# Optimization experiments

Hardware: AMD Instinct MI355X
Metric: run time of the kernel (lower is better)

Reference implementation:

```python
import jax, jax.numpy as jnp
import numpy as np

B, S, D, H = 1, 4096, 768, 12
HD = D // H
FF = 4 * D
EPS = 1e-5


def _layer_norm(x, w, b):
    mu = jnp.mean(x, axis=-1, keepdims=True)
    var = jnp.mean((x - mu) ** 2, axis=-1, keepdims=True)
    return (x - mu) * jax.lax.rsqrt(var + EPS) * w + b


def setup_inputs() -> dict:
    key = jax.random.key(0)
    ks = jax.random.split(key, 16)
    s = 0.02
    inp = {
        "hidden_states": jax.random.normal(ks[0], (B, S, D), jnp.float32),
        "attention_mask": jnp.ones((B, S), jnp.int32),
        "ln1_w": jnp.ones((D,), jnp.float32),
        "ln1_b": jnp.zeros((D,), jnp.float32),
        "wq": jax.random.normal(ks[1], (D, D), jnp.float32) * s,
        "bq": jnp.zeros((D,), jnp.float32),
        "wk": jax.random.normal(ks[2], (D, D), jnp.float32) * s,
        "bk": jnp.zeros((D,), jnp.float32),
        "wv": jax.random.normal(ks[3], (D, D), jnp.float32) * s,
        "bv": jnp.zeros((D,), jnp.float32),
        "wo": jax.random.normal(ks[4], (D, D), jnp.float32) * s,
        "bo": jnp.zeros((D,), jnp.float32),
        "ln2_w": jnp.ones((D,), jnp.float32),
        "ln2_b": jnp.zeros((D,), jnp.float32),
        "w_up": jax.random.normal(ks[5], (D, FF), jnp.float32) * s,
        "b_up": jnp.zeros((FF,), jnp.float32),
        "w_down": jax.random.normal(ks[6], (FF, D), jnp.float32) * s,
        "b_down": jnp.zeros((D,), jnp.float32),
    }
    return inp


def reference(hidden_states, attention_mask, ln1_w, ln1_b, wq, bq, wk, bk, wv, bv,
              wo, bo, ln2_w, ln2_b, w_up, b_up, w_down, b_down):
    b, s, _ = hidden_states.shape
    residual = hidden_states
    x = _layer_norm(hidden_states, ln1_w, ln1_b)
    # projections; weights stored [in, out]
    q = (x @ wq + bq).reshape(b, s, H, HD).transpose(0, 2, 1, 3)  # (b,h,s,hd)
    k = (x @ wk + bk).reshape(b, s, H, HD).transpose(0, 2, 1, 3)
    v = (x @ wv + bv).reshape(b, s, H, HD).transpose(0, 2, 1, 3)
    scores = jnp.einsum("bhqd,bhkd->bhqk", q, k) / np.float32(np.sqrt(HD))
    causal = jnp.triu(jnp.ones((s, s), bool), k=1)  # True above diagonal -> mask
    neg_inf = jnp.float32(-jnp.inf)
    scores = jnp.where(causal[None, None, :, :], neg_inf, scores)
    pad = (attention_mask[:, None, None, :] == 0)
    scores = jnp.where(pad, neg_inf, scores)
    weights = jax.nn.softmax(scores, axis=-1)
    attn = jnp.einsum("bhqk,bhkd->bhqd", weights, v)
    attn = attn.transpose(0, 2, 1, 3).reshape(b, s, D)
    hidden = residual + (attn @ wo + bo)
    # FFN
    residual = hidden
    y = _layer_norm(hidden, ln2_w, ln2_b)
    y = jax.nn.gelu(y @ w_up + b_up, approximate=False)
    y = y @ w_down + b_down
    return residual + y
```

## Files before the change

### kernel.cpp

```cpp
#include <hip/hip_runtime.h>
#include <cstdint>
#include <cstddef>


#define S_  4096
#define D_  768
#define H_  12
#define HD_ 64
#define FF_ 3072
#define SD_ (4096 * 768)

typedef short  short8  __attribute__((ext_vector_type(8)));
typedef float  floatx4 __attribute__((ext_vector_type(4)));

__device__ __forceinline__ float bf2f(unsigned short h) {
  union { unsigned int u; float f; } v; v.u = ((unsigned int)h) << 16; return v.f;
}
__device__ __forceinline__ unsigned short f2bf(float f) {
  union { unsigned int u; float f; } v; v.f = f;
  unsigned int u = v.u;
  return (unsigned short)((u + 0x7FFFu + ((u >> 16) & 1u)) >> 16);
}
__device__ __forceinline__ unsigned short f2bf_fast(float f) {
  union { unsigned int u; float f; } v; v.f = f;
  return (unsigned short)((v.u + 0x8000u) >> 16);
}
__device__ __forceinline__ void gload_lds16(const unsigned short* g, unsigned short* l) {
  __builtin_amdgcn_global_load_lds(
      (const __attribute__((address_space(1))) unsigned int*)g,
      (__attribute__((address_space(3))) unsigned int*)l, 16, 0, 0);
}

__global__ void k_cvt_f32(const void* __restrict__ src, float* __restrict__ dst,
                          int n, const int* __restrict__ flagp) {
  const int flag = *flagp;
  for (int i = blockIdx.x * blockDim.x + threadIdx.x; i < n; i += gridDim.x * blockDim.x)
    dst[i] = flag ? ((const float*)src)[i] : bf2f(((const unsigned short*)src)[i]);
}

__global__ __launch_bounds__(256) void k_cvt_t6(
    const void* s0, const void* s1, const void* s2, const void* s3,
    const void* s4, const void* s5,
    unsigned short* d0, unsigned short* d1, unsigned short* d2,
    unsigned short* d3, unsigned short* d4, unsigned short* d5,
    const int* __restrict__ flagp) {
  __shared__ unsigned short T[64 * 65];
  const int flag = *flagp;
  const int b = blockIdx.x;
  const void* src; unsigned short* dst; int K, N, ti;
  if (b < 576) {
    const int seg = b / 144; ti = b - seg * 144; K = 768; N = 768;
    const void* ss[4] = {s0, s1, s2, s3};
    unsigned short* dd[4] = {d0, d1, d2, d3};
    src = ss[seg]; dst = dd[seg];
  } else if (b < 1152) { ti = b - 576;  K = 768;  N = 3072; src = s4; dst = d4; }
  else                 { ti = b - 1152; K = 3072; N = 768;  src = s5; dst = d5; }
  const int nx = N >> 6;
  const int n0 = (ti % nx) * 64, k0 = (ti / nx) * 64;
  const int t = threadIdx.x;
  const int cl = t & 63, rg = t >> 6;
#pragma unroll
  for (int i = 0; i < 16; ++i) {
    const int kl = rg * 16 + i;
    const size_t si = (size_t)(k0 + kl) * N + n0 + cl;
    T[kl * 65 + cl] = flag ? f2bf(((const float*)src)[si]) : ((const unsigned short*)src)[si];
  }
  __syncthreads();
#pragma unroll
  for (int i = 0; i < 16; ++i) {
    const int nl = rg * 16 + i;
    dst[(size_t)(n0 + nl) * K + k0 + cl] = T[cl * 65 + nl];
  }
}

__global__ void k_cvt_params(const void* p0, const void* p1, const void* p2, const void* p3,
                             const void* p4, const void* p5, const void* p6, const void* p7,
                             const void* p8, const void* p9,
                             float* __restrict__ dst, int* __restrict__ flagp) {
  const int flag = (((const unsigned int*)p0)[0] == 0x3F800000u) ? 1 : 0;
  int i = blockIdx.x * 256 + threadIdx.x;
  if (i == 0) *flagp = flag;
  if (i >= 9984) return;
  const void* src; int j;
  if (i < 6912) {
    int seg = i / 768; j = i - seg * 768;
    const void* tbl[9] = {p0, p1, p2, p3, p4, p5, p6, p7, p8};
    src = tbl[seg];
  } else { src = p9; j = i - 6912; }
  dst[i] = flag ? ((const float*)src)[j] : bf2f(((const unsigned short*)src)[j]);
}

__global__ __launch_bounds__(256) void k_ln(const float* __restrict__ x,
                                            const float* __restrict__ w,
                                            const float* __restrict__ b,
                                            unsigned short* __restrict__ out) {
  const int row = blockIdx.x, t = threadIdx.x;
  const float* xr = x + (size_t)row * D_;
  float v0 = xr[t], v1 = xr[t + 256], v2 = xr[t + 512];
  float s = v0 + v1 + v2;
  float ss = v0 * v0 + v1 * v1 + v2 * v2;
  for (int off = 32; off > 0; off >>= 1) {
    s  += __shfl_down(s, off);
    ss += __shfl_down(ss, off);
  }
  __shared__ float sb[4], ssb[4];
  const int wid = t >> 6, lane = t & 63;
  if (lane == 0) { sb[wid] = s; ssb[wid] = ss; }
  __syncthreads();
  s  = sb[0] + sb[1] + sb[2] + sb[3];
  ss = ssb[0] + ssb[1] + ssb[2] + ssb[3];
  const float mu   = s * (1.0f / D_);
  const float var  = ss * (1.0f / D_) - mu * mu;
  const float rstd = rsqrtf(var + 1e-5f);
  unsigned short* orow = out + (size_t)row * D_;
  orow[t]       = f2bf((v0 - mu) * rstd * w[t]       + b[t]);
  orow[t + 256] = f2bf((v1 - mu) * rstd * w[t + 256] + b[t + 256]);
  orow[t + 512] = f2bf((v2 - mu) * rstd * w[t + 512] + b[t + 512]);
}

template <int TBM, int TBN>
__global__ __launch_bounds__(256) void k_gemm_t(
    const unsigned short* __restrict__ A, const unsigned short* __restrict__ Wt,
    const float* __restrict__ bias, const float* __restrict__ resid,
    void* __restrict__ Cout, int M, int N, int K, int mode, const int* __restrict__ flagp) {
  constexpr int MI = TBM / 32, MJ = TBN / 32;
  __shared__ __align__(16) unsigned short As[TBM * 32];
  __shared__ __align__(16) unsigned short Bs[TBN * 32];
  const int t = threadIdx.x;
  const int w = t >> 6, lane = t & 63;
  const int quad = lane >> 4, l16 = lane & 15;
  const int mb = blockIdx.y * TBM, nb = blockIdx.x * TBN;
  const int wm = (w >> 1) * (TBM / 2), wn = (w & 1) * (TBN / 2);
  const int grow = lane >> 2;
  const int gcol = (lane & 3) * 8;

  floatx4 acc[MI][MJ];
#pragma unroll
  for (int i = 0; i < MI; ++i)
#pragma unroll
    for (int j = 0; j < MJ; ++j) acc[i][j] = (floatx4){0.f, 0.f, 0.f, 0.f};

  for (int k0 = 0; k0 < K; k0 += 32) {
    __syncthreads();
#pragma unroll
    for (int r = 0; r < TBM / 64; ++r) {
      const int ch = r * 4 + w;
      gload_lds16(A + (size_t)(mb + ch * 16 + grow) * K + k0 + gcol, &As[ch * 512]);
    }
#pragma unroll
    for (int r = 0; r < TBN / 64; ++r) {
      const int ch = r * 4 + w;
      gload_lds16(Wt + (size_t)(nb + ch * 16 + grow) * K + k0 + gcol, &Bs[ch * 512]);
    }
    __syncthreads();

    union { short8 v; uint4 q; } fa[MI], fb[MJ];
#pragma unroll
    for (int i = 0; i < MI; ++i)
      fa[i].q = *(const uint4*)&As[(wm + i * 16 + l16) * 32 + quad * 8];
#pragma unroll
    for (int j = 0; j < MJ; ++j)
      fb[j].q = *(const uint4*)&Bs[(wn + j * 16 + l16) * 32 + quad * 8];
#pragma unroll
    for (int i = 0; i < MI; ++i)
#pragma unroll
      for (int j = 0; j < MJ; ++j)
        acc[i][j] = __builtin_amdgcn_mfma_f32_16x16x32_bf16(fa[i].v, fb[j].v, acc[i][j], 0, 0, 0);
  }

  const int flag = (mode == 3) ? *flagp : 0;
#pragma unroll
  for (int i = 0; i < MI; ++i) {
#pragma unroll
    for (int j = 0; j < MJ; ++j) {
      const int col = nb + wn + j * 16 + l16;
      const float bv = bias[col];
#pragma unroll
      for (int r = 0; r < 4; ++r) {
        const int row = mb + wm + i * 16 + quad * 4 + r;
        const size_t idx = (size_t)row * N + col;
        float v = acc[i][j][r] + bv;
        if (mode == 0) {
          ((unsigned short*)Cout)[idx] = f2bf(v);
        } else if (mode == 1) {
          ((float*)Cout)[idx] = v + resid[idx];
        } else if (mode == 2) {
          float g = 0.5f * v * (1.0f + erff(v * 0.70710678118f));
          ((unsigned short*)Cout)[idx] = f2bf(g);
        } else if (mode == 5) {
          unsigned short* q = (unsigned short*)Cout;
          if (col < 768)        q[(size_t)row * 768 + col] = f2bf(v);
          else if (col < 1536) (q + SD_)[(size_t)row * 768 + col - 768] = f2bf(v);
          else                 (q + 2 * (size_t)SD_)[(size_t)(col - 1536) * 4096 + row] = f2bf(v);
        } else {
          v += resid[idx];
          if (flag) ((float*)Cout)[idx] = v;
          else      ((unsigned short*)Cout)[idx] = f2bf(v);
        }
      }
    }
  }
}

#define LK 72
__global__ __launch_bounds__(256) void k_attn_chunk(
    const unsigned short* __restrict__ qb, const unsigned short* __restrict__ kb,
    const unsigned short* __restrict__ vtb, const int* __restrict__ amask,
    unsigned short* __restrict__ Opart, float* __restrict__ Lpart) {
  const int h = blockIdx.y, x = blockIdx.x;
  int g, base;
  if (x < 8)       { g = 0; base = 0; }
  else if (x < 24) { g = 1; base = 8; }
  else if (x < 48) { g = 2; base = 24; }
  else             { g = 3; base = 48; }
  const int rem = x - base;
  const int qt = 8 * g + rem / (g + 1);
  const int c  = rem % (g + 1);
  const int qbase = qt * 128;
  const int kt0 = c * 16;
  const int kt1 = min(kt0 + 16, 2 * qt + 2);

  __shared__ __align__(16) unsigned short Kt[64 * LK];
  __shared__ __align__(16) unsigned short Vt[64 * LK];
  __shared__ __align__(16) unsigned short Ps[128 * LK];
  __shared__ int Mk[64];
  const int t = threadIdx.x;
  const int w = t >> 6, lane = t & 63;
  const int quad = lane >> 4, l16 = lane & 15;
  const int sr = t >> 2, sc = (t & 3) * 16;

  union { short8 v; uint4 q; } qf[2][2];
#pragma unroll
  for (int sub = 0; sub < 2; ++sub) {
    const unsigned short* qp =
        qb + (size_t)(qbase + w * 32 + sub * 16 + l16) * D_ + h * HD_ + quad * 8;
    qf[sub][0].q = *(const uint4*)qp;
    qf[sub][1].q = *(const uint4*)(qp + 32);
  }
  short8 onesB;
#pragma unroll
  for (int e = 0; e < 8; ++e) onesB[e] = (short)0x3F80;
  unsigned short* myP = &Ps[w * 32 * LK];

  floatx4 O[2][4], Lacc[2];
#pragma unroll
  for (int sub = 0; sub < 2; ++sub) {
    Lacc[sub] = (floatx4){0.f, 0.f, 0.f, 0.f};
#pragma unroll
    for (int dc = 0; dc < 4; ++dc) O[sub][dc] = (floatx4){0.f, 0.f, 0.f, 0.f};
  }
  const float sscale = 0.125f * 1.4426950408889634f;
  const int qrow0 = qbase + w * 32 + quad * 4;

  for (int kt = kt0; kt < kt1; ++kt) {
    const int kbase = kt * 64;
    __syncthreads();
    {
      const unsigned short* ks = kb + (size_t)(kbase + sr) * D_ + h * HD_ + sc;
      *(uint4*)&Kt[sr * LK + sc]     = *(const uint4*)ks;
      *(uint4*)&Kt[sr * LK + sc + 8] = *(const uint4*)(ks + 8);
      const unsigned short* vs = vtb + (size_t)(h * HD_ + sr) * S_ + kbase + sc;
      *(uint4*)&Vt[sr * LK + sc]     = *(const uint4*)vs;
      *(uint4*)&Vt[sr * LK + sc + 8] = *(const uint4*)(vs + 8);
      if (t < 64) Mk[t] = amask[kbase + t];
    }
    __syncthreads();

    const bool diag = (kt >= 2 * qt);
#pragma unroll
    for (int kc = 0; kc < 4; ++kc) {
      union { short8 v; uint4 q; } kf[2];
      const unsigned short* p0 = &Kt[(kc * 16 + l16) * LK + quad * 8];
      kf[0].q = *(const uint4*)p0;
      kf[1].q = *(const uint4*)(p0 + 32);
      floatx4 cc[2];
#pragma unroll
      for (int sub = 0; sub < 2; ++sub) {
        cc[sub] = (floatx4){0.f, 0.f, 0.f, 0.f};
        cc[sub] = __builtin_amdgcn_mfma_f32_16x16x32_bf16(qf[sub][0].v, kf[0].v, cc[sub], 0, 0, 0);
        cc[sub] = __builtin_amdgcn_mfma_f32_16x16x32_bf16(qf[sub][1].v, kf[1].v, cc[sub], 0, 0, 0);
      }
      const float mb = (Mk[kc * 16 + l16] == 0) ? -127.f : 0.f;
      const int kg = kbase + kc * 16 + l16;
#pragma unroll
      for (int sub = 0; sub < 2; ++sub)
#pragma unroll
        for (int r = 0; r < 4; ++r) {
          float sv = cc[sub][r] * sscale + mb;
          if (diag && kg > qrow0 + sub * 16 + r) sv = -127.f;
          myP[(sub * 16 + quad * 4 + r) * LK + kc * 16 + l16] = f2bf_fast(exp2f(sv));
        }
    }
    union { short8 v; uint4 q; } pf[2][2];
#pragma unroll
    for (int sub = 0; sub < 2; ++sub) {
      const unsigned short* p0 = &myP[(sub * 16 + l16) * LK + quad * 8];
      pf[sub][0].q = *(const uint4*)p0;
      pf[sub][1].q = *(const uint4*)(p0 + 32);
      Lacc[sub] = __builtin_amdgcn_mfma_f32_16x16x32_bf16(pf[sub][0].v, onesB, Lacc[sub], 0, 0, 0);
      Lacc[sub] = __builtin_amdgcn_mfma_f32_16x16x32_bf16(pf[sub][1].v, onesB, Lacc[sub], 0, 0, 0);
    }
#pragma unroll
    for (int dc = 0; dc < 4; ++dc) {
      union { short8 v; uint4 q; } vf[2];
      const unsigned short* p0 = &Vt[(dc * 16 + l16) * LK + quad * 8];
      vf[0].q = *(const uint4*)p0;
      vf[1].q = *(const uint4*)(p0 + 32);
#pragma unroll
      for (int sub = 0; sub < 2; ++sub) {
        O[sub][dc] = __builtin_amdgcn_mfma_f32_16x16x32_bf16(pf[sub][0].v, vf[0].v, O[sub][dc], 0, 0, 0);
        O[sub][dc] = __builtin_amdgcn_mfma_f32_16x16x32_bf16(pf[sub][1].v, vf[1].v, O[sub][dc], 0, 0, 0);
      }
    }
  }

  const size_t slot = (size_t)h * 80 + x;
#pragma unroll
  for (int sub = 0; sub < 2; ++sub) {
#pragma unroll
    for (int dc = 0; dc < 4; ++dc)
#pragma unroll
      for (int r = 0; r < 4; ++r)
        Opart[slot * 8192 + (w * 32 + sub * 16 + quad * 4 + r) * 64 + dc * 16 + l16] =
            f2bf(O[sub][dc][r]);
    if (l16 == 0) {
#pragma unroll
      for (int r = 0; r < 4; ++r)
        Lpart[slot * 128 + w * 32 + sub * 16 + quad * 4 + r] = Lacc[sub][r];
    }
  }
}

__global__ __launch_bounds__(256) void k_attn_merge(
    const unsigned short* __restrict__ Opart, const float* __restrict__ Lpart,
    unsigned short* __restrict__ ob) {
  const int qt = blockIdx.x, h = blockIdx.y;
  const int t = threadIdx.x;
  const int row = t >> 1, half = (t & 1) * 32;
  const int g = qt >> 3;
  const int nch = g + 1;
  const int cb = h * 80 + 4 * g * (g + 1) + (qt & 7) * (g + 1);
  float L = 0.f;
  float acc[32];
#pragma unroll
  for (int j = 0; j < 32; ++j) acc[j] = 0.f;
  for (int ci = 0; ci < nch; ++ci) {
    L += Lpart[(size_t)(cb + ci) * 128 + row];
    const unsigned short* op = Opart + (size_t)(cb + ci) * 8192 + row * 64 + half;
#pragma unroll
    for (int j4 = 0; j4 < 4; ++j4) {
      union { uint4 v; unsigned short e[8]; } u;
      u.v = *(const uint4*)(op + j4 * 8);
#pragma unroll
      for (int e = 0; e < 8; ++e) acc[j4 * 8 + e] += bf2f(u.e[e]);
    }
  }
  const float inv = 1.f / L;
  unsigned short* orow = ob + (size_t)(qt * 128 + row) * D_ + h * HD_ + half;
#pragma unroll
  for (int j4 = 0; j4 < 4; ++j4) {
    union { uint4 v; unsigned short e[8]; } u;
#pragma unroll
    for (int e = 0; e < 8; ++e) u.e[e] = f2bf(acc[j4 * 8 + e] * inv);
    *(uint4*)(orow + j4 * 8) = u.v;
  }
}

extern "C" void kernel_launch(void* const* d_in, const int* in_sizes, int n_in,
                              void* d_out, int out_size, void* d_ws, size_t ws_size,
                              hipStream_t stream) {
  const void* hidden = d_in[0];
  const int*  amask  = (const int*)d_in[1];
  const void* ln1w = d_in[2];  const void* ln1b = d_in[3];
  const void* wq   = d_in[4];  const void* bq   = d_in[5];
  const void* wk   = d_in[6];  const void* bk   = d_in[7];
  const void* wv   = d_in[8];  const void* bv   = d_in[9];
  const void* wo   = d_in[10]; const void* bo   = d_in[11];
  const void* ln2w = d_in[12]; const void* ln2b = d_in[13];
  const void* wup  = d_in[14]; const void* bup  = d_in[15];
  const void* wdn  = d_in[16]; const void* bdn  = d_in[17];

  char* ws = (char*)d_ws;
  size_t off = 0;
  auto alloc = [&](size_t bytes) {
    char* p = ws + off;
    off += (bytes + 255) & ~(size_t)255;
    return p;
  };
  const size_t SD = (size_t)SD_;
  int*            flagp = (int*)alloc(4);
  float*          h1    = (float*)alloc(SD * 4);
  float*          prm   = (float*)alloc(9984 * 4);
  float*          h2    = (float*)alloc(SD * 4);
  unsigned short* xb    = (unsigned short*)alloc(SD * 2);
  unsigned short* wqkvt = (unsigned short*)alloc((size_t)2304 * 768 * 2);
  unsigned short* wot   = (unsigned short*)alloc((size_t)768 * 768 * 2);
  unsigned short* wupt  = (unsigned short*)alloc((size_t)3072 * 768 * 2);
  unsigned short* wdnt  = (unsigned short*)alloc((size_t)768 * 3072 * 2);
  unsigned short* big   = (unsigned short*)alloc((size_t)S_ * FF_ * 2);
  unsigned short* qb2 = big;
  unsigned short* kb2 = big + SD;
  unsigned short* vtb = big + 2 * SD;
  unsigned short* ab  = big + 3 * SD;
  unsigned short* ffb = big;
  unsigned short* Opart = (unsigned short*)h2;
  float*          Lpart = (float*)((char*)h2 + (size_t)960 * 8192 * 2);

  float* f_ln1w = prm;        float* f_ln1b = prm + 768;
  float* f_ln2w = prm + 1536; float* f_ln2b = prm + 2304;
  float* f_bqkv = prm + 3072; float* f_bo = prm + 5376;
  float* f_bdn = prm + 6144;  float* f_bup = prm + 6912;

  k_cvt_params<<<39, 256, 0, stream>>>(ln1w, ln1b, ln2w, ln2b, bq, bk, bv, bo, bdn, bup,
                                       prm, flagp);
  k_cvt_f32<<<1024, 256, 0, stream>>>(hidden, h1, (int)SD, flagp);
  k_cvt_t6<<<1728, 256, 0, stream>>>(wq, wk, wv, wo, wup, wdn,
                                     wqkvt, wqkvt + 768 * 768, wqkvt + 2 * 768 * 768,
                                     wot, wupt, wdnt, flagp);

  k_ln<<<S_, 256, 0, stream>>>(h1, f_ln1w, f_ln1b, xb);

  k_gemm_t<128, 128><<<dim3(18, 32), 256, 0, stream>>>(
      xb, wqkvt, f_bqkv, nullptr, qb2, S_, 2304, 768, 5, flagp);

  k_attn_chunk<<<dim3(80, 12), 256, 0, stream>>>(qb2, kb2, vtb, amask, Opart, Lpart);
  k_attn_merge<<<dim3(32, 12), 256, 0, stream>>>(Opart, Lpart, ab);

  k_gemm_t<128, 64><<<dim3(12, 32), 256, 0, stream>>>(
      ab, wot, f_bo, h1, h2, S_, 768, 768, 1, flagp);

  k_ln<<<S_, 256, 0, stream>>>(h2, f_ln2w, f_ln2b, xb);

  k_gemm_t<128, 128><<<dim3(24, 32), 256, 0, stream>>>(
      xb, wupt, f_bup, nullptr, ffb, S_, 3072, 768, 2, flagp);
  k_gemm_t<128, 64><<<dim3(12, 32), 256, 0, stream>>>(
      ffb, wdnt, f_bdn, h2, d_out, S_, 768, 3072, 3, flagp);
}
```

Before: 406.0 us.

## Split-K the down-projection GEMM with atomic accumulation into a residual-initialized buffer

The down-projection GEMM (K=3072) now runs with a 4-way split-K grid. Each slice atomically adds its partial result into an fp32 buffer that the second LayerNorm kernel pre-fills with residual plus bias. A new small kernel then converts that buffer to the output dtype. The aim is to raise occupancy from 384 blocks to 1536 on a long-K GEMM, at the cost of atomic traffic, an extra pass over the output, and non-deterministic summation order.

```diff
diff --git a/kernel.cpp b/kernel.cpp
--- a/kernel.cpp
+++ b/kernel.cpp
@@ -93,7 +93,9 @@
 __global__ __launch_bounds__(256) void k_ln(const float* __restrict__ x,
                                             const float* __restrict__ w,
                                             const float* __restrict__ b,
-                                            unsigned short* __restrict__ out) {
+                                            unsigned short* __restrict__ out,
+                                            const float* __restrict__ bias2,
+                                            float* __restrict__ acc) {
   const int row = blockIdx.x, t = threadIdx.x;
   const float* xr = x + (size_t)row * D_;
   float v0 = xr[t], v1 = xr[t + 256], v2 = xr[t + 512];
@@ -116,6 +118,12 @@
   orow[t]       = f2bf((v0 - mu) * rstd * w[t]       + b[t]);
   orow[t + 256] = f2bf((v1 - mu) * rstd * w[t + 256] + b[t + 256]);
   orow[t + 512] = f2bf((v2 - mu) * rstd * w[t + 512] + b[t + 512]);
+  if (acc) {
+    float* arow = acc + (size_t)row * D_;
+    arow[t]       = v0 + bias2[t];
+    arow[t + 256] = v1 + bias2[t + 256];
+    arow[t + 512] = v2 + bias2[t + 512];
+  }
 }
 
 template <int TBM, int TBN>
@@ -140,7 +148,9 @@
 #pragma unroll
     for (int j = 0; j < MJ; ++j) acc[i][j] = (floatx4){0.f, 0.f, 0.f, 0.f};
 
-  for (int k0 = 0; k0 < K; k0 += 32) {
+  const int kpb = K / gridDim.z;
+  const int kb0 = kpb * blockIdx.z;
+  for (int k0 = kb0; k0 < kb0 + kpb; k0 += 32) {
     __syncthreads();
 #pragma unroll
     for (int r = 0; r < TBM / 64; ++r) {
@@ -174,7 +184,7 @@
 #pragma unroll
     for (int j = 0; j < MJ; ++j) {
       const int col = nb + wn + j * 16 + l16;
-      const float bv = bias[col];
+      const float bv = (mode == 6) ? 0.f : bias[col];
 #pragma unroll
       for (int r = 0; r < 4; ++r) {
         const int row = mb + wm + i * 16 + quad * 4 + r;
@@ -192,6 +202,8 @@
           if (col < 768)        q[(size_t)row * 768 + col] = f2bf(v);
           else if (col < 1536) (q + SD_)[(size_t)row * 768 + col - 768] = f2bf(v);
           else                 (q + 2 * (size_t)SD_)[(size_t)(col - 1536) * 4096 + row] = f2bf(v);
+        } else if (mode == 6) {
+          unsafeAtomicAdd((float*)Cout + idx, v);
         } else {
           v += resid[idx];
           if (flag) ((float*)Cout)[idx] = v;
@@ -199,6 +211,21 @@
         }
       }
     }
+  }
+}
+
+__global__ __launch_bounds__(256) void k_out(const float* __restrict__ acc,
+                                             const int* __restrict__ flagp,
+                                             void* __restrict__ out) {
+  const int i = (blockIdx.x * 256 + threadIdx.x) * 4;
+  const floatx4 v = *(const floatx4*)(acc + i);
+  if (*flagp) {
+    *(floatx4*)((float*)out + i) = v;
+  } else {
+    union { unsigned short e[4]; uint2 u; } p;
+#pragma unroll
+    for (int e = 0; e < 4; ++e) p.e[e] = f2bf(v[e]);
+    *(uint2*)((unsigned short*)out + i) = p.u;
   }
 }
 
@@ -418,7 +445,7 @@
                                      wqkvt, wqkvt + 768 * 768, wqkvt + 2 * 768 * 768,
                                      wot, wupt, wdnt, flagp);
 
-  k_ln<<<S_, 256, 0, stream>>>(h1, f_ln1w, f_ln1b, xb);
+  k_ln<<<S_, 256, 0, stream>>>(h1, f_ln1w, f_ln1b, xb, nullptr, nullptr);
 
   k_gemm_t<128, 128><<<dim3(18, 32), 256, 0, stream>>>(
       xb, wqkvt, f_bqkv, nullptr, qb2, S_, 2304, 768, 5, flagp);
@@ -429,10 +456,13 @@
   k_gemm_t<128, 64><<<dim3(12, 32), 256, 0, stream>>>(
       ab, wot, f_bo, h1, h2, S_, 768, 768, 1, flagp);
 
-  k_ln<<<S_, 256, 0, stream>>>(h2, f_ln2w, f_ln2b, xb);
+  k_ln<<<S_, 256, 0, stream>>>(h2, f_ln2w, f_ln2b, xb, f_bdn, h1);
 
   k_gemm_t<128, 128><<<dim3(24, 32), 256, 0, stream>>>(
       xb, wupt, f_bup, nullptr, ffb, S_, 3072, 768, 2, flagp);
-  k_gemm_t<128, 64><<<dim3(12, 32), 256, 0, stream>>>(
-      ffb, wdnt, f_bdn, h2, d_out, S_, 768, 3072, 3, flagp);
-}
+
+  k_gemm_t<128, 64><<<dim3(12, 32, 4), 256, 0, stream>>>(
+      ffb, wdnt, nullptr, nullptr, h1, S_, 768, 3072, 6, flagp);
+
+  k_out<<<3072, 256, 0, stream>>>(h1, flagp, d_out);
+}
```

Result: slower. 416.5 us (+2.6%).
